# Performance work log

Hardware: AMD Instinct MI355X
Metric: run time of the kernel (lower is better)

Reference implementation:

```python
import jax, jax.numpy as jnp
import numpy as np

N_NODES = 50000


def gcn_conv(x, W, b, src, dst, n_nodes):
    """PyG GCNConv: h = x @ W; symmetric-normalized aggregation with self-loops; + bias."""
    h = x @ W  # [N, F_out]
    ones = jnp.ones(src.shape[0], dtype=h.dtype)
    # degree including the self-loop (edge weight 1)
    deg = jax.ops.segment_sum(ones, dst, num_segments=n_nodes) + 1.0
    dinv = jax.lax.rsqrt(deg)  # deg >= 1, always valid
    norm = dinv[src] * dinv[dst]  # [E]
    msgs = h[src] * norm[:, None]  # [E, F_out]
    agg = jax.ops.segment_sum(msgs, dst, num_segments=n_nodes)
    agg = agg + h * (dinv * dinv)[:, None]  # self-loop contribution, norm = dinv_i^2
    return agg + b


def setup_inputs() -> dict:
    key = jax.random.key(0)
    ks = jax.random.split(key, 8)
    n, f_in, f_hid, f_out, n_edges = N_NODES, 128, 128, 40, 800000
    x = jax.random.normal(ks[0], (n, f_in), dtype=jnp.float32)
    edge_index = jax.random.randint(ks[1], (2, n_edges), 0, n, dtype=jnp.int64)
    new_edge_indexs = jax.random.randint(ks[2], (2, 1000), 0, n, dtype=jnp.int64)
    # Glorot init like PyG defaults
    s1 = (6.0 / (f_in + f_hid)) ** 0.5
    s2 = (6.0 / (f_hid + f_out)) ** 0.5
    W1 = jax.random.uniform(ks[3], (f_in, f_hid), jnp.float32, -s1, s1)
    b1 = jnp.zeros((f_hid,), jnp.float32)
    W2 = jax.random.uniform(ks[4], (f_hid, f_out), jnp.float32, -s2, s2)
    b2 = jnp.zeros((f_out,), jnp.float32)
    return {"x": x, "W1": W1, "b1": b1, "W2": W2, "b2": b2,
            "edge_index": edge_index, "new_edge_indexs": new_edge_indexs}


def reference(x, W1, b1, W2, b2, edge_index, new_edge_indexs):
    src, dst = edge_index[0], edge_index[1]
    h = gcn_conv(x, W1, b1, src, dst, N_NODES)
    h = jax.nn.relu(h)
    # dropout(p=0.5) is identity in eval mode (training=False)
    h = gcn_conv(h, W2, b2, src, dst, N_NODES)
    return jax.nn.log_softmax(h, axis=-1)
```

## Files before the change

### kernel.cpp

```cpp
#include <hip/hip_runtime.h>
#include <hip/hip_bf16.h>

#define N_NODES 50000
#define N_EDGES 800000
#define F_IN    128
#define F_HID   128
#define F_OUT   40
#define N_TILES (N_NODES / 16)

#define NBIN      98
#define BIN_SHIFT 9
#define EPB       1024
#define CAP       32
#define GBIN_CAP  9216

#define CVT_BLOCKS ((F_IN * F_HID + 48 * F_HID) / 256)
#define BIN_BLOCKS ((N_EDGES + EPB - 1) / EPB)
#define G1_BLOCKS  ((N_TILES + 3) / 4)

typedef __attribute__((ext_vector_type(8))) short bf16x8;
typedef __attribute__((ext_vector_type(4))) float f32x4;

__device__ __forceinline__ float2 unpack_bf2(unsigned u) {
    float2 r;
    r.x = __uint_as_float(u << 16);
    r.y = __uint_as_float(u & 0xffff0000u);
    return r;
}
__device__ __forceinline__ unsigned pack_bf2(float x, float y) {
    union { unsigned u; __hip_bfloat16 h[2]; } cv;
    cv.h[0] = __float2bfloat16(x);
    cv.h[1] = __float2bfloat16(y);
    return cv.u;
}
__device__ __forceinline__ short bfraw(float v) {
    __hip_bfloat16 h = __float2bfloat16(v);
    return *(short*)&h;
}
__device__ __forceinline__ float bf16u_to_f32(unsigned short us) {
    return __uint_as_float(((unsigned)us) << 16);
}
__device__ __forceinline__ unsigned f32_to_h16(float v) {
    _Float16 h = (_Float16)v;
    return (unsigned)*(unsigned short*)&h;
}
__device__ __forceinline__ float h16_to_f32(unsigned bits) {
    unsigned short us = (unsigned short)bits;
    _Float16 h = *(_Float16*)&us;
    return (float)h;
}

__device__ __forceinline__ int ld_src(const unsigned int* w, int is64, int e) {
    return is64 ? (int)w[2 * e] : (int)w[e];
}
__device__ __forceinline__ int ld_dst(const unsigned int* w, int is64, int e) {
    return is64 ? (int)w[2 * (N_EDGES + e)] : (int)w[N_EDGES + e];
}

__global__ void k_init(const unsigned int* __restrict__ ew,
                       const float* __restrict__ W1, const float* __restrict__ W2,
                       __hip_bfloat16* __restrict__ w1t, __hip_bfloat16* __restrict__ w2t,
                       int* __restrict__ flag, int* __restrict__ gcnt) {
    int b = blockIdx.x, t = threadIdx.x;
    if (b < CVT_BLOCKS) {
        int idx = b * 256 + t;
        if (idx < F_IN * F_HID) {
            int n = idx >> 7, k = idx & 127;
            w1t[idx] = __float2bfloat16(W1[k * F_HID + n]);
        } else {
            int j = idx - F_IN * F_HID;
            int n = j >> 7, k = j & 127;
            w2t[j] = __float2bfloat16(n < F_OUT ? W2[k * F_OUT + n] : 0.f);
        }
        return;
    }
    __shared__ int nz;
    if (t == 0) nz = 0;
    __syncthreads();
    int local = 0;
    for (int i = t; i < 4096; i += 256)
        if (ew[2 * i + 1] != 0u) local = 1;
    if (local) atomicOr(&nz, 1);
    if (t < NBIN) gcnt[t] = 0;
    __syncthreads();
    if (t == 0) flag[0] = (nz == 0) ? 1 : 0;
}

__global__ void k_bing1(const unsigned int* __restrict__ ew, const int* __restrict__ flag,
                        int* __restrict__ gcnt, unsigned* __restrict__ gbin,
                        const float* __restrict__ x, const __hip_bfloat16* __restrict__ w1t,
                        __hip_bfloat16* __restrict__ h1b) {
    __shared__ unsigned buf[NBIN][CAP];
    __shared__ int cnt[NBIN];
    __shared__ int base[NBIN];
    int t = threadIdx.x;
    if (blockIdx.x < BIN_BLOCKS) {
        for (int i = t; i < NBIN; i += 256) cnt[i] = 0;
        __syncthreads();
        int is64 = flag[0];
        int e0 = blockIdx.x * EPB;
        int n = min(EPB, N_EDGES - e0);
        for (int i = t; i < n; i += 256) {
            int e = e0 + i;
            int s = ld_src(ew, is64, e), d = ld_dst(ew, is64, e);
            unsigned rec = (unsigned)s | ((unsigned)d << 16);
            int b = d >> BIN_SHIFT;
            int c = atomicAdd(&cnt[b], 1);
            if (c < CAP) buf[b][c] = rec;
            else {
                int g = atomicAdd(&gcnt[b], 1);
                gbin[(size_t)b * GBIN_CAP + g] = rec;
            }
        }
        __syncthreads();
        if (t < NBIN) {
            int m = min(cnt[t], CAP);
            base[t] = atomicAdd(&gcnt[t], m);
            cnt[t] = m;
        }
        __syncthreads();
        int wave = t >> 6, lane = t & 63;
        for (int b = wave; b < NBIN; b += 4) {
            int m = cnt[b], bs = base[b];
            for (int i = lane; i < m; i += 64)
                gbin[(size_t)b * GBIN_CAP + bs + i] = buf[b][i];
        }
        return;
    }
    int wave = t >> 6, lane = t & 63;
    int tile = (blockIdx.x - BIN_BLOCKS) * 4 + wave;
    if (tile >= N_TILES) return;
    int node0 = tile * 16;
    int m = lane & 15, q = lane >> 4;
    bf16x8 A[4];
    const float* arow = x + (size_t)(node0 + m) * F_IN + q * 8;
#pragma unroll
    for (int kt = 0; kt < 4; kt++) {
        float4 f0 = *(const float4*)(arow + kt * 32);
        float4 f1 = *(const float4*)(arow + kt * 32 + 4);
        bf16x8 a;
        a[0] = bfraw(f0.x); a[1] = bfraw(f0.y); a[2] = bfraw(f0.z); a[3] = bfraw(f0.w);
        a[4] = bfraw(f1.x); a[5] = bfraw(f1.y); a[6] = bfraw(f1.z); a[7] = bfraw(f1.w);
        A[kt] = a;
    }
#pragma unroll
    for (int c = 0; c < 8; c++) {
        f32x4 acc = {0.f, 0.f, 0.f, 0.f};
        const __hip_bfloat16* brow = w1t + (size_t)(c * 16 + m) * F_IN + q * 8;
#pragma unroll
        for (int kt = 0; kt < 4; kt++) {
            bf16x8 B = *(const bf16x8*)(brow + kt * 32);
            acc = __builtin_amdgcn_mfma_f32_16x16x32_bf16(A[kt], B, acc, 0, 0, 0);
        }
#pragma unroll
        for (int r = 0; r < 4; r++)
            h1b[(size_t)(node0 + q * 4 + r) * F_HID + c * 16 + m] = __float2bfloat16(acc[r]);
    }
}

__global__ void k_passB1(const int* __restrict__ gcnt, const unsigned* __restrict__ gbin,
                         int* __restrict__ rowptr, float* __restrict__ dinv) {
    __shared__ int c[512];
    __shared__ int s2[256];
    __shared__ int gall[NBIN];
    __shared__ int bbase;
    int t = threadIdx.x;
    int b = blockIdx.x;
    c[t] = 0; c[t + 256] = 0;
    if (t < NBIN) gall[t] = gcnt[t];
    __syncthreads();
    if (t == 0) {
        int s = 0;
        for (int i = 0; i < b; i++) s += gall[i];
        bbase = s;
    }
    int n = gall[b];
    const unsigned* rec = gbin + (size_t)b * GBIN_CAP;
    int base512 = b << BIN_SHIFT;
    for (int i = t; i < n; i += 256)
        atomicAdd(&c[(int)(rec[i] >> 16) - base512], 1);
    __syncthreads();
    int a0 = c[2 * t], a1 = c[2 * t + 1];
    s2[t] = a0 + a1;
    __syncthreads();
    for (int off = 1; off < 256; off <<= 1) {
        int u = (t >= off) ? s2[t - off] : 0;
        __syncthreads();
        s2[t] += u;
        __syncthreads();
    }
    int ebase = bbase + s2[t] - a0 - a1;
    int i0 = base512 + 2 * t, i1 = i0 + 1;
    if (i0 < N_NODES) { rowptr[i0] = ebase;      dinv[i0] = rsqrtf((float)a0 + 1.f); }
    if (i1 < N_NODES) { rowptr[i1] = ebase + a0; dinv[i1] = rsqrtf((float)a1 + 1.f); }
    if (b == 0 && t == 0) rowptr[N_NODES] = N_EDGES;
}

__global__ void k_passB2(const int* __restrict__ gcnt, const unsigned* __restrict__ gbin,
                         const int* __restrict__ rowptr, const float* __restrict__ dinv,
                         unsigned* __restrict__ srcw) {
    __shared__ int pos[512];
    __shared__ float dloc[512];
    int t = threadIdx.x;
    int b = blockIdx.x;
    int base512 = b << BIN_SHIFT;
#pragma unroll
    for (int k = 0; k < 2; k++) {
        int j = t + k * 256;
        int i = base512 + j;
        pos[j]  = (i < N_NODES) ? rowptr[i] : 0;
        dloc[j] = (i < N_NODES) ? dinv[i] : 0.f;
    }
    __syncthreads();
    int n = gcnt[b];
    const unsigned* rec = gbin + (size_t)b * GBIN_CAP;
    for (int i = t; i < n; i += 256) {
        unsigned r = rec[i];
        int s  = (int)(r & 0xFFFFu);
        int dl = (int)(r >> 16) - base512;
        int slot = atomicAdd(&pos[dl], 1);
        float norm = dinv[s] * dloc[dl];
        srcw[slot] = (unsigned)s | (f32_to_h16(norm) << 16);
    }
}

__global__ void k_agg1f(const int* __restrict__ rowptr, const unsigned* __restrict__ srcw,
                        const float* __restrict__ dinv, const __hip_bfloat16* __restrict__ h1b,
                        const float* __restrict__ b1, __hip_bfloat16* __restrict__ h1rb) {
    int wave = threadIdx.x >> 6, lane = threadIdx.x & 63;
    int node = blockIdx.x * 4 + wave;
    float di = dinv[node];
    int beg = __builtin_amdgcn_readfirstlane(rowptr[node]);
    int end = __builtin_amdgcn_readfirstlane(rowptr[node + 1]);
    const unsigned* h1u = (const unsigned*)h1b;
    float2 acc = unpack_bf2(h1u[(size_t)node * 64 + lane]);
    float w0 = di * di;
    acc.x *= w0; acc.y *= w0;
    int e = beg;
    for (; e + 7 < end; e += 8) {
        unsigned p[8];
#pragma unroll
        for (int j = 0; j < 8; j++) p[j] = srcw[e + j];
        unsigned u[8];
#pragma unroll
        for (int j = 0; j < 8; j++)
            u[j] = h1u[(size_t)(p[j] & 0xFFFFu) * 64 + lane];
#pragma unroll
        for (int j = 0; j < 8; j++) {
            float w = h16_to_f32(p[j] >> 16);
            float2 v = unpack_bf2(u[j]);
            acc.x += v.x * w;
            acc.y += v.y * w;
        }
    }
    for (; e < end; e++) {
        unsigned p = srcw[e];
        float w = h16_to_f32(p >> 16);
        float2 v = unpack_bf2(h1u[(size_t)(p & 0xFFFFu) * 64 + lane]);
        acc.x += v.x * w;
        acc.y += v.y * w;
    }
    float2 bb = ((const float2*)b1)[lane];
    acc.x = fmaxf(acc.x + bb.x, 0.f);
    acc.y = fmaxf(acc.y + bb.y, 0.f);
    ((unsigned*)h1rb)[(size_t)node * 64 + lane] = pack_bf2(acc.x, acc.y);
}

__global__ void k_gemm2m(const __hip_bfloat16* __restrict__ h1rb,
                         const __hip_bfloat16* __restrict__ w2t,
                         __hip_bfloat16* __restrict__ h2b) {
    int wave = threadIdx.x >> 6, lane = threadIdx.x & 63;
    int tile = blockIdx.x * 4 + wave;
    if (tile >= N_TILES) return;
    int node0 = tile * 16;
    int m = lane & 15, q = lane >> 4;
    bf16x8 A[4];
    const __hip_bfloat16* arow = h1rb + (size_t)(node0 + m) * F_HID + q * 8;
#pragma unroll
    for (int kt = 0; kt < 4; kt++)
        A[kt] = *(const bf16x8*)(arow + kt * 32);
#pragma unroll
    for (int c = 0; c < 3; c++) {
        f32x4 acc = {0.f, 0.f, 0.f, 0.f};
        const __hip_bfloat16* brow = w2t + (size_t)(c * 16 + m) * F_HID + q * 8;
#pragma unroll
        for (int kt = 0; kt < 4; kt++) {
            bf16x8 B = *(const bf16x8*)(brow + kt * 32);
            acc = __builtin_amdgcn_mfma_f32_16x16x32_bf16(A[kt], B, acc, 0, 0, 0);
        }
        int col = c * 16 + m;
        if (col < F_OUT) {
#pragma unroll
            for (int r = 0; r < 4; r++)
                h2b[(size_t)(node0 + q * 4 + r) * F_OUT + col] = __float2bfloat16(acc[r]);
        }
    }
}

__global__ void k_agg2f(const int* __restrict__ rowptr, const unsigned* __restrict__ srcw,
                        const float* __restrict__ dinv,
                        const unsigned short* __restrict__ h2b,
                        const float* __restrict__ b2, float* __restrict__ out) {
    int wave = threadIdx.x >> 6, lane = threadIdx.x & 63;
    int node = blockIdx.x * 4 + wave;
    float di = dinv[node];
    int beg = __builtin_amdgcn_readfirstlane(rowptr[node]);
    int end = __builtin_amdgcn_readfirstlane(rowptr[node + 1]);
    int l = (lane < F_OUT) ? lane : 0;
    float acc = bf16u_to_f32(h2b[(size_t)node * F_OUT + l]) * di * di;
    int e = beg;
    for (; e + 7 < end; e += 8) {
        unsigned p[8];
#pragma unroll
        for (int j = 0; j < 8; j++) p[j] = srcw[e + j];
        float v[8];
#pragma unroll
        for (int j = 0; j < 8; j++)
            v[j] = bf16u_to_f32(h2b[(size_t)(p[j] & 0xFFFFu) * F_OUT + l]);
#pragma unroll
        for (int j = 0; j < 8; j++)
            acc += v[j] * h16_to_f32(p[j] >> 16);
    }
    for (; e < end; e++) {
        unsigned p = srcw[e];
        acc += bf16u_to_f32(h2b[(size_t)(p & 0xFFFFu) * F_OUT + l]) * h16_to_f32(p >> 16);
    }
    float v = (lane < F_OUT) ? acc + b2[lane] : -INFINITY;
    float m = v;
    for (int off = 32; off; off >>= 1) m = fmaxf(m, __shfl_xor(m, off));
    float ex = (lane < F_OUT) ? __expf(v - m) : 0.f;
    float ssum = ex;
    for (int off = 32; off; off >>= 1) ssum += __shfl_xor(ssum, off);
    float ls = __logf(ssum);
    if (lane < F_OUT)
        out[(size_t)node * F_OUT + lane] = v - m - ls;
}

extern "C" void kernel_launch(void* const* d_in, const int* in_sizes, int n_in,
                              void* d_out, int out_size, void* d_ws, size_t ws_size,
                              hipStream_t stream) {
    const float* x  = (const float*)d_in[0];
    const float* W1 = (const float*)d_in[1];
    const float* b1 = (const float*)d_in[2];
    const float* W2 = (const float*)d_in[3];
    const float* b2 = (const float*)d_in[4];
    const unsigned int* ew = (const unsigned int*)d_in[5];
    float* out = (float*)d_out;

    char* ws = (char*)d_ws;
    int*   flag     = (int*)ws;   ws += 256;
    int*   gcnt     = (int*)ws;   ws += 512;
    float* dinv     = (float*)ws; ws += ((N_NODES * 4 + 255) / 256) * 256;
    int*   rowptr   = (int*)ws;   ws += (((N_NODES + 1) * 4 + 255) / 256) * 256;
    unsigned* gbin  = (unsigned*)ws; ws += (size_t)NBIN * GBIN_CAP * 4;
    unsigned* srcw  = (unsigned*)ws; ws += (size_t)N_EDGES * 4;
    __hip_bfloat16* w1t  = (__hip_bfloat16*)ws; ws += F_IN * F_HID * 2;
    __hip_bfloat16* w2t  = (__hip_bfloat16*)ws; ws += 48 * F_HID * 2;
    __hip_bfloat16* h1b  = (__hip_bfloat16*)ws; ws += (size_t)N_NODES * F_HID * 2;
    __hip_bfloat16* h1rb = (__hip_bfloat16*)ws; ws += (size_t)N_NODES * F_HID * 2;
    __hip_bfloat16* h2b  = (__hip_bfloat16*)ws; ws += (size_t)N_NODES * F_OUT * 2;

    k_init   <<<CVT_BLOCKS + 1, 256, 0, stream>>>(ew, W1, W2, w1t, w2t, flag, gcnt);
    k_bing1  <<<BIN_BLOCKS + G1_BLOCKS, 256, 0, stream>>>(ew, flag, gcnt, gbin, x, w1t, h1b);
    k_passB1 <<<NBIN, 256, 0, stream>>>(gcnt, gbin, rowptr, dinv);
    k_passB2 <<<NBIN, 256, 0, stream>>>(gcnt, gbin, rowptr, dinv, srcw);
    k_agg1f  <<<N_NODES / 4, 256, 0, stream>>>(rowptr, srcw, dinv, h1b, b1, h1rb);
    k_gemm2m <<<(N_TILES + 3) / 4, 256, 0, stream>>>(h1rb, w2t, h2b);
    k_agg2f  <<<N_NODES / 4, 256, 0, stream>>>(rowptr, srcw, dinv,
                                               (const unsigned short*)h2b, b2, out);
}
```

Measured before the change: 209.3 us.

## Fuse second-layer GEMM into first aggregation kernel via shared-memory FP32 dot products

The layer-1 aggregation kernel now writes its relu'd 128-wide node rows into shared memory and, after a block barrier, computes the 40-column layer-2 projection with scalar FP32 dot products against a transposed FP32 W2. This removes the separate MFMA GEMM kernel, one launch, and the write and read-back of the intermediate bf16 hidden matrix. In exchange it adds a __syncthreads to the latency-bound gather kernel and does the small GEMM on vector ALUs, with W2 rows fetched per thread from cache, which uses only 40 of 64 lanes per wave.

```diff
diff --git a/kernel.cpp b/kernel.cpp
--- a/kernel.cpp
+++ b/kernel.cpp
@@ -14,7 +14,8 @@
 #define CAP       32
 #define GBIN_CAP  9216
 
-#define CVT_BLOCKS ((F_IN * F_HID + 48 * F_HID) / 256)
+#define CVT_ELEMS (F_IN * F_HID + F_OUT * F_HID)
+#define CVT_BLOCKS (CVT_ELEMS / 256)
 #define BIN_BLOCKS ((N_EDGES + EPB - 1) / EPB)
 #define G1_BLOCKS  ((N_TILES + 3) / 4)
 
@@ -27,12 +28,6 @@
     r.y = __uint_as_float(u & 0xffff0000u);
     return r;
 }
-__device__ __forceinline__ unsigned pack_bf2(float x, float y) {
-    union { unsigned u; __hip_bfloat16 h[2]; } cv;
-    cv.h[0] = __float2bfloat16(x);
-    cv.h[1] = __float2bfloat16(y);
-    return cv.u;
-}
 __device__ __forceinline__ short bfraw(float v) {
     __hip_bfloat16 h = __float2bfloat16(v);
     return *(short*)&h;
@@ -59,7 +54,7 @@
 
 __global__ void k_init(const unsigned int* __restrict__ ew,
                        const float* __restrict__ W1, const float* __restrict__ W2,
-                       __hip_bfloat16* __restrict__ w1t, __hip_bfloat16* __restrict__ w2t,
+                       __hip_bfloat16* __restrict__ w1t, float* __restrict__ w2tf,
                        int* __restrict__ flag, int* __restrict__ gcnt) {
     int b = blockIdx.x, t = threadIdx.x;
     if (b < CVT_BLOCKS) {
@@ -70,7 +65,7 @@
         } else {
             int j = idx - F_IN * F_HID;
             int n = j >> 7, k = j & 127;
-            w2t[j] = __float2bfloat16(n < F_OUT ? W2[k * F_OUT + n] : 0.f);
+            w2tf[j] = W2[k * F_OUT + n];
         }
         return;
     }
@@ -224,9 +219,11 @@
     }
 }
 
-__global__ void k_agg1f(const int* __restrict__ rowptr, const unsigned* __restrict__ srcw,
-                        const float* __restrict__ dinv, const __hip_bfloat16* __restrict__ h1b,
-                        const float* __restrict__ b1, __hip_bfloat16* __restrict__ h1rb) {
+__global__ void k_agg1g2(const int* __restrict__ rowptr, const unsigned* __restrict__ srcw,
+                         const float* __restrict__ dinv, const __hip_bfloat16* __restrict__ h1b,
+                         const float* __restrict__ b1, const float* __restrict__ w2tf,
+                         __hip_bfloat16* __restrict__ h2b) {
+    __shared__ float xs[4][F_HID];
     int wave = threadIdx.x >> 6, lane = threadIdx.x & 63;
     int node = blockIdx.x * 4 + wave;
     float di = dinv[node];
@@ -261,39 +258,20 @@
         acc.y += v.y * w;
     }
     float2 bb = ((const float2*)b1)[lane];
-    acc.x = fmaxf(acc.x + bb.x, 0.f);
-    acc.y = fmaxf(acc.y + bb.y, 0.f);
-    ((unsigned*)h1rb)[(size_t)node * 64 + lane] = pack_bf2(acc.x, acc.y);
-}
-
-__global__ void k_gemm2m(const __hip_bfloat16* __restrict__ h1rb,
-                         const __hip_bfloat16* __restrict__ w2t,
-                         __hip_bfloat16* __restrict__ h2b) {
-    int wave = threadIdx.x >> 6, lane = threadIdx.x & 63;
-    int tile = blockIdx.x * 4 + wave;
-    if (tile >= N_TILES) return;
-    int node0 = tile * 16;
-    int m = lane & 15, q = lane >> 4;
-    bf16x8 A[4];
-    const __hip_bfloat16* arow = h1rb + (size_t)(node0 + m) * F_HID + q * 8;
-#pragma unroll
-    for (int kt = 0; kt < 4; kt++)
-        A[kt] = *(const bf16x8*)(arow + kt * 32);
-#pragma unroll
-    for (int c = 0; c < 3; c++) {
-        f32x4 acc = {0.f, 0.f, 0.f, 0.f};
-        const __hip_bfloat16* brow = w2t + (size_t)(c * 16 + m) * F_HID + q * 8;
-#pragma unroll
-        for (int kt = 0; kt < 4; kt++) {
-            bf16x8 B = *(const bf16x8*)(brow + kt * 32);
-            acc = __builtin_amdgcn_mfma_f32_16x16x32_bf16(A[kt], B, acc, 0, 0, 0);
-        }
-        int col = c * 16 + m;
-        if (col < F_OUT) {
-#pragma unroll
-            for (int r = 0; r < 4; r++)
-                h2b[(size_t)(node0 + q * 4 + r) * F_OUT + col] = __float2bfloat16(acc[r]);
-        }
+    xs[wave][2 * lane]     = fmaxf(acc.x + bb.x, 0.f);
+    xs[wave][2 * lane + 1] = fmaxf(acc.y + bb.y, 0.f);
+    __syncthreads();
+    int nd = threadIdx.x >> 6, col = threadIdx.x & 63;
+    if (col < F_OUT) {
+        const float4* wrow = (const float4*)(w2tf + col * F_HID);
+        const float4* xrow = (const float4*)xs[nd];
+        float s = 0.f;
+#pragma unroll 8
+        for (int k = 0; k < F_HID / 4; k++) {
+            float4 a = xrow[k], w = wrow[k];
+            s += a.x * w.x + a.y * w.y + a.z * w.z + a.w * w.w;
+        }
+        h2b[(size_t)(blockIdx.x * 4 + nd) * F_OUT + col] = __float2bfloat16(s);
     }
 }
 
@@ -354,18 +332,16 @@
     int*   rowptr   = (int*)ws;   ws += (((N_NODES + 1) * 4 + 255) / 256) * 256;
     unsigned* gbin  = (unsigned*)ws; ws += (size_t)NBIN * GBIN_CAP * 4;
     unsigned* srcw  = (unsigned*)ws; ws += (size_t)N_EDGES * 4;
-    __hip_bfloat16* w1t  = (__hip_bfloat16*)ws; ws += F_IN * F_HID * 2;
-    __hip_bfloat16* w2t  = (__hip_bfloat16*)ws; ws += 48 * F_HID * 2;
-    __hip_bfloat16* h1b  = (__hip_bfloat16*)ws; ws += (size_t)N_NODES * F_HID * 2;
-    __hip_bfloat16* h1rb = (__hip_bfloat16*)ws; ws += (size_t)N_NODES * F_HID * 2;
-    __hip_bfloat16* h2b  = (__hip_bfloat16*)ws; ws += (size_t)N_NODES * F_OUT * 2;
-
-    k_init   <<<CVT_BLOCKS + 1, 256, 0, stream>>>(ew, W1, W2, w1t, w2t, flag, gcnt);
+    __hip_bfloat16* w1t = (__hip_bfloat16*)ws; ws += F_IN * F_HID * 2;
+    float* w2tf = (float*)ws;     ws += F_OUT * F_HID * 4;
+    __hip_bfloat16* h1b = (__hip_bfloat16*)ws; ws += (size_t)N_NODES * F_HID * 2;
+    __hip_bfloat16* h2b = (__hip_bfloat16*)ws; ws += (size_t)N_NODES * F_OUT * 2;
+
+    k_init   <<<CVT_BLOCKS + 1, 256, 0, stream>>>(ew, W1, W2, w1t, w2tf, flag, gcnt);
     k_bing1  <<<BIN_BLOCKS + G1_BLOCKS, 256, 0, stream>>>(ew, flag, gcnt, gbin, x, w1t, h1b);
     k_passB1 <<<NBIN, 256, 0, stream>>>(gcnt, gbin, rowptr, dinv);
     k_passB2 <<<NBIN, 256, 0, stream>>>(gcnt, gbin, rowptr, dinv, srcw);
-    k_agg1f  <<<N_NODES / 4, 256, 0, stream>>>(rowptr, srcw, dinv, h1b, b1, h1rb);
-    k_gemm2m <<<(N_TILES + 3) / 4, 256, 0, stream>>>(h1rb, w2t, h2b);
+    k_agg1g2 <<<N_NODES / 4, 256, 0, stream>>>(rowptr, srcw, dinv, h1b, b1, w2tf, h2b);
     k_agg2f  <<<N_NODES / 4, 256, 0, stream>>>(rowptr, srcw, dinv,
                                                (const unsigned short*)h2b, b2, out);
 }
```

Result: slower. 314.1 us (+50.1%).
